# Kernel optimization log

Hardware: AMD Instinct MI355X
Metric: run time of the kernel (lower is better)

Reference implementation:

```python
import jax, jax.numpy as jnp
import numpy as np

N, IN_DIM, HEADS, OUT_DIM = 100000, 128, 4, 32
E = 1600000
NEG_SLOPE = 0.2

def setup_inputs() -> dict:
    key = jax.random.key(0)
    k1, k2, k3, k4, k5 = jax.random.split(key, 5)
    x = jax.random.normal(k1, (N, IN_DIM), dtype=jnp.float32)
    edge_index = jax.random.randint(k2, (2, E), 0, N, dtype=jnp.int32)
    # xavier-like init for params
    W = jax.random.uniform(k3, (IN_DIM, HEADS * OUT_DIM), dtype=jnp.float32,
                           minval=-1.0, maxval=1.0) * np.sqrt(6.0 / (IN_DIM + HEADS * OUT_DIM))
    a_src = jax.random.uniform(k4, (HEADS, OUT_DIM), dtype=jnp.float32,
                               minval=-1.0, maxval=1.0) * np.sqrt(6.0 / (HEADS + OUT_DIM))
    a_dst = jax.random.uniform(k5, (HEADS, OUT_DIM), dtype=jnp.float32,
                               minval=-1.0, maxval=1.0) * np.sqrt(6.0 / (HEADS + OUT_DIM))
    return {"x": x, "edge_index": edge_index, "W": W, "a_src": a_src, "a_dst": a_dst}

def reference(x, edge_index, W, a_src, a_dst):
    src, dst = edge_index[0], edge_index[1]
    n = x.shape[0]
    h = (x @ W).reshape(n, HEADS, OUT_DIM)                      # (N,H,D)
    # per-node attention score halves, then gather per edge (avoids E x D gather twice)
    s_src = jnp.einsum('nhd,hd->nh', h, a_src)                  # (N,H)
    s_dst = jnp.einsum('nhd,hd->nh', h, a_dst)                  # (N,H)
    e = s_src[src] + s_dst[dst]                                 # (E,H)
    e = jnp.where(e > 0, e, NEG_SLOPE * e)                      # leaky_relu(0.2)
    # segment softmax over edges sharing the same dst, per head
    max_per_dst = jax.ops.segment_max(e, dst, num_segments=n)   # (N,H)
    exp = jnp.exp(e - max_per_dst[dst])                         # (E,H)
    denom = jax.ops.segment_sum(exp, dst, num_segments=n)       # (N,H)
    alpha = exp / (denom[dst] + 1e-9)                           # (E,H)
    msg = h[src] * alpha[:, :, None]                            # (E,H,D)
    out = jax.ops.segment_sum(msg, dst, num_segments=n)         # (N,H,D)
    return out.reshape(n, HEADS * OUT_DIM)                      # concat=True
```

## Files before the change

kernel.cpp:

```cpp
#include <hip/hip_runtime.h>
#include <hip/hip_bf16.h>
#include <stdint.h>

#define N_NODES 100000
#define NE 1600000
#define NEG_SLOPE 0.2f
#define NSTRIP 6250
#define NGROUP 49
#define GCAP 34816
#define NFB 64
#define NBKT 3136
#define CAP 768
#define NCTR (NGROUP * 32 + NBKT)

typedef __attribute__((ext_vector_type(8))) short bf16x8;
typedef __attribute__((ext_vector_type(4))) float f32x4;
typedef __attribute__((ext_vector_type(2))) float f32x2;
typedef __attribute__((ext_vector_type(4))) uint32_t u32x4;
typedef __attribute__((ext_vector_type(2))) uint32_t u32x2;

__device__ __forceinline__ short f2bf(float f) {
    __hip_bfloat16 b = __float2bfloat16(f);
    short s; __builtin_memcpy(&s, &b, 2); return s;
}

__global__ __launch_bounds__(256) void k_prep(const float* __restrict__ W,
                                              const float* __restrict__ a_src,
                                              const float* __restrict__ a_dst,
                                              float* __restrict__ vv,
                                              short* __restrict__ wbf,
                                              int* __restrict__ ctrs) {
    const int t = threadIdx.x;
    if (blockIdx.x == 0) {
        if (t < 128) {
            const float* wrow = W + t * 128;
            #pragma unroll
            for (int hd = 0; hd < 4; ++hd) {
                float va = 0.f, vd = 0.f;
                #pragma unroll
                for (int d = 0; d < 32; ++d) {
                    float w = wrow[hd * 32 + d];
                    va += w * a_src[hd * 32 + d];
                    vd += w * a_dst[hd * 32 + d];
                }
                vv[t * 8 + hd]     = va;
                vv[t * 8 + 4 + hd] = vd;
            }
        }
        #pragma unroll 4
        for (int i = 0; i < 64; ++i) {
            int idx = t + i * 256;
            int k = idx >> 7, c = idx & 127;
            int byte = ((c << 8) + (k << 1)) ^ ((c & 7) << 4);
            *(short*)((char*)wbf + byte) = f2bf(W[idx]);
        }
    } else {
        for (int i = t; i < NCTR; i += 256) ctrs[i] = 0;
    }
}

__global__ __launch_bounds__(256) void k_gemm(const float* __restrict__ x,
                                              const short* __restrict__ wbf,
                                              const float* __restrict__ vv,
                                              unsigned char* __restrict__ h8,
                                              float* __restrict__ scales,
                                              float* __restrict__ sv) {
    __shared__ short wt[16384];
    __shared__ float vvl[1024];
    __shared__ float sc[64];
    const int t = threadIdx.x;

    {
        const int4* wsrc = (const int4*)wbf;
        int4* wdst = (int4*)wt;
        #pragma unroll
        for (int i = 0; i < 8; ++i) wdst[t + i * 256] = wsrc[t + i * 256];
    }
    *(f32x4*)(vvl + t * 4) = *(const f32x4*)(vv + t * 4);
    __syncthreads();

    const int wid = t >> 6, lane = t & 63;
    const int strip = blockIdx.x * 4 + wid;
    const bool active = strip < NSTRIP;
    const int r0 = strip * 16;
    const int lr = lane & 15, lg = lane >> 4;

    f32x4 acc[8];
    #pragma unroll
    for (int ct = 0; ct < 8; ++ct) acc[ct] = (f32x4){0.f, 0.f, 0.f, 0.f};
    float part[8];
    #pragma unroll
    for (int i = 0; i < 8; ++i) part[i] = 0.f;

    if (active) {
        bf16x8 a[4];
        #pragma unroll
        for (int kk = 0; kk < 4; ++kk) {
            const float* xp = x + (size_t)(r0 + lr) * 128 + kk * 32 + lg * 8;
            f32x4 x0 = *(const f32x4*)xp;
            f32x4 x1 = *(const f32x4*)(xp + 4);
            int kbase = kk * 32 + lg * 8;
            #pragma unroll
            for (int j = 0; j < 4; ++j) {
                a[kk][j]     = f2bf(x0[j]);
                a[kk][4 + j] = f2bf(x1[j]);
                f32x4 v0 = *(const f32x4*)(vvl + (kbase + j) * 8);
                f32x4 v1 = *(const f32x4*)(vvl + (kbase + j) * 8 + 4);
                f32x4 w0 = *(const f32x4*)(vvl + (kbase + 4 + j) * 8);
                f32x4 w1 = *(const f32x4*)(vvl + (kbase + 4 + j) * 8 + 4);
                #pragma unroll
                for (int i = 0; i < 4; ++i) {
                    part[i]     += x0[j] * v0[i] + x1[j] * w0[i];
                    part[4 + i] += x0[j] * v1[i] + x1[j] * w1[i];
                }
            }
        }
        #pragma unroll
        for (int ct = 0; ct < 8; ++ct) {
            int c = ct * 16 + lr;
            #pragma unroll
            for (int kk = 0; kk < 4; ++kk) {
                int byte = ((c << 8) + ((kk * 32 + lg * 8) << 1)) ^ ((c & 7) << 4);
                bf16x8 b = *(const bf16x8*)((char*)wt + byte);
                acc[ct] = __builtin_amdgcn_mfma_f32_16x16x32_bf16(a[kk], b, acc[ct], 0, 0, 0);
            }
        }
    }
    #pragma unroll
    for (int i = 0; i < 8; ++i) {
        part[i] += __shfl_xor(part[i], 16);
        part[i] += __shfl_xor(part[i], 32);
    }
    if (active && lg == 0) {
        f32x4 s0, s1;
        #pragma unroll
        for (int j = 0; j < 4; ++j) { s0[j] = part[j]; s1[j] = part[4 + j]; }
        *(f32x4*)(sv + (size_t)(r0 + lr) * 8)     = s0;
        *(f32x4*)(sv + (size_t)(r0 + lr) * 8 + 4) = s1;
    }
    if (active) {
        #pragma unroll
        for (int j = 0; j < 4; ++j) {
            float rm = 0.f;
            #pragma unroll
            for (int ct = 0; ct < 8; ++ct) rm = fmaxf(rm, fabsf(acc[ct][j]));
            #pragma unroll
            for (int off2 = 1; off2 < 16; off2 <<= 1)
                rm = fmaxf(rm, __shfl_xor(rm, off2));
            if (lr == 0) {
                scales[r0 + lg * 4 + j] = rm * (1.f / 127.f);
                sc[wid * 16 + lg * 4 + j] = 127.f / fmaxf(rm, 1e-20f);
            }
        }
    }
    __syncthreads();
    if (active) {
        #pragma unroll
        for (int ct = 0; ct < 8; ++ct) {
            #pragma unroll
            for (int j = 0; j < 4; ++j) {
                int row = wid * 16 + lg * 4 + j;
                wt[row * 128 + ct * 16 + lr] = f2bf(acc[ct][j]);
            }
        }
    }
    __syncthreads();
    const int R0 = blockIdx.x * 64;
    #pragma unroll
    for (int it = 0; it < 2; ++it) {
        int sidx = (it * 256 + t) * 16;
        int lrow = sidx >> 7, ch0 = sidx & 127;
        int grow = R0 + lrow;
        if (grow < N_NODES) {
            float invs = sc[lrow];
            u32x4 dws;
            #pragma unroll
            for (int d = 0; d < 4; ++d) {
                uint32_t dw = 0;
                #pragma unroll
                for (int bb = 0; bb < 4; ++bb) {
                    union { uint32_t i; float f; } uu;
                    uu.i = ((uint32_t)(uint16_t)wt[sidx + d * 4 + bb]) << 16;
                    float q = rintf(uu.f * invs);
                    q = fminf(fmaxf(q, -127.f), 127.f);
                    dw |= ((uint32_t)(int)(q + 128.f)) << (8 * bb);
                }
                dws[d] = dw;
            }
            *(u32x4*)(h8 + (size_t)grow * 128 + ch0) = dws;
        }
    }
}

__global__ __launch_bounds__(256) void k_part1(const int* __restrict__ ei,
                                               int* __restrict__ gcur,
                                               int* __restrict__ arena) {
    __shared__ int hist[NGROUP];
    __shared__ int lstart[NGROUP + 1];
    __shared__ int gb[NGROUP];
    __shared__ int binned[4096];
    const int t = threadIdx.x;
    const int e4b = blockIdx.x * 1024;
    if (t < NGROUP) hist[t] = 0;
    __syncthreads();
    int pk[16], gr[16], pl[16];
    #pragma unroll
    for (int i = 0; i < 4; ++i) {
        int e4 = e4b + i * 256 + t;
        bool v = e4 < NE / 4;
        int4 s4 = {0, 0, 0, 0}, d4 = {0, 0, 0, 0};
        if (v) {
            s4 = *(const int4*)(ei + (size_t)e4 * 4);
            d4 = *(const int4*)(ei + NE + (size_t)e4 * 4);
        }
#define P1(k, sf, df) { \
        if (v) { int g = (df) >> 11; gr[i*4+k] = g; \
                 pk[i*4+k] = ((sf) << 11) | ((df) & 2047); \
                 pl[i*4+k] = atomicAdd(&hist[g], 1); } else gr[i*4+k] = -1; }
        P1(0, s4.x, d4.x) P1(1, s4.y, d4.y) P1(2, s4.z, d4.z) P1(3, s4.w, d4.w)
#undef P1
    }
    __syncthreads();
    if (t < 64) {
        int v = (t < NGROUP) ? hist[t] : 0;
        int incl = v;
        #pragma unroll
        for (int off = 1; off < 64; off <<= 1) {
            int y = __shfl_up(incl, off);
            if (t >= off) incl += y;
        }
        if (t < NGROUP) lstart[t + 1] = incl;
        if (t == 0) lstart[0] = 0;
    }
    __syncthreads();
    if (t < NGROUP) gb[t] = atomicAdd(&gcur[t * 32], hist[t]);
    #pragma unroll
    for (int j = 0; j < 16; ++j)
        if (gr[j] >= 0) binned[lstart[gr[j]] + pl[j]] = pk[j];
    __syncthreads();
    const int lane = t & 63, wid = t >> 6;
    for (int g = wid; g < NGROUP; g += 4) {
        int base = gb[g];
        int n = min(hist[g], GCAP - base);
        const int ls = lstart[g];
        int* dst = arena + (size_t)g * GCAP + base;
        for (int i = lane; i < n; i += 64) dst[i] = binned[ls + i];
    }
}

__global__ __launch_bounds__(256) void k_part2(const int* __restrict__ gcur,
                                               const int* __restrict__ arena,
                                               int* __restrict__ bcur,
                                               int* __restrict__ tmp2) {
    const int g = blockIdx.x / 9, chunk = blockIdx.x - g * 9;
    const int cnt = min(gcur[g * 32], GCAP);
    const int cb = chunk * 4096;
    if (cb >= cnt) return;
    __shared__ int hist[NFB];
    __shared__ int lstart[NFB + 1];
    __shared__ int gb[NFB];
    __shared__ int binned[4096];
    const int t = threadIdx.x;
    if (t < NFB) hist[t] = 0;
    __syncthreads();
    int pk[16], fb[16], pl[16];
    const int* ga = arena + (size_t)g * GCAP;
    #pragma unroll
    for (int i = 0; i < 4; ++i) {
        int i4 = cb / 4 + i * 256 + t;
        bool v4 = (i4 * 4) < cnt;
        int4 w4 = {0, 0, 0, 0};
        if (v4) w4 = *(const int4*)(ga + (size_t)i4 * 4);
#define P2(k, wf) { int idx = i4 * 4 + k; \
        if (v4 && idx < cnt) { int f = ((wf) & 2047) >> 5; fb[i*4+k] = f; \
            pk[i*4+k] = (((wf) >> 11) << 5) | ((wf) & 31); \
            pl[i*4+k] = atomicAdd(&hist[f], 1); } else fb[i*4+k] = -1; }
        P2(0, w4.x) P2(1, w4.y) P2(2, w4.z) P2(3, w4.w)
#undef P2
    }
    __syncthreads();
    if (t < 64) {
        int v = hist[t];
        int incl = v;
        #pragma unroll
        for (int off = 1; off < 64; off <<= 1) {
            int y = __shfl_up(incl, off);
            if (t >= off) incl += y;
        }
        lstart[t + 1] = incl;
        if (t == 0) lstart[0] = 0;
    }
    __syncthreads();
    if (t < NFB) gb[t] = atomicAdd(&bcur[g * 64 + t], hist[t]);
    #pragma unroll
    for (int j = 0; j < 16; ++j)
        if (fb[j] >= 0) binned[lstart[fb[j]] + pl[j]] = pk[j];
    __syncthreads();
    const int lane = t & 63, wid = t >> 6;
    for (int f = wid; f < NFB; f += 4) {
        int base = gb[f];
        int n = min(hist[f], CAP - base);
        const int ls = lstart[f];
        int* dst = tmp2 + (size_t)(g * 64 + f) * CAP + base;
        for (int i = lane; i < n; i += 64) dst[i] = binned[ls + i];
    }
}

__global__ __launch_bounds__(256) void k_aggregate(const unsigned char* __restrict__ h8,
                                                   const float* __restrict__ scales,
                                                   const float* __restrict__ sv,
                                                   const int* __restrict__ bcur,
                                                   const int* __restrict__ tmp2,
                                                   float* __restrict__ out) {
    const int b = blockIdx.x;
    const int base = (b >> 6) * 2048 + (b & 63) * 32;
    if (base >= N_NODES) return;
    __shared__ int sorted[CAP];
    __shared__ float wbuf[CAP * 4];
    __shared__ float sbuf[CAP];
    __shared__ int cstart[33];
    __shared__ int ccnt[32];
    __shared__ f32x4 svd4[32];
    const int t = threadIdx.x;
    if (t < 32) {
        ccnt[t] = 0;
        svd4[t] = *(const f32x4*)(sv + (size_t)(base + t) * 8 + 4);
    }
    __syncthreads();
    const int cnt = min(bcur[b], CAP);
    const int* mytmp = tmp2 + (size_t)b * CAP;
    int e0 = -1, e1 = -1, e2 = -1, q0 = 0, q1 = 0, q2 = 0;
    if (t < cnt)       { e0 = mytmp[t];       q0 = atomicAdd(&ccnt[e0 & 31], 1); }
    if (t + 256 < cnt) { e1 = mytmp[t + 256]; q1 = atomicAdd(&ccnt[e1 & 31], 1); }
    if (t + 512 < cnt) { e2 = mytmp[t + 512]; q2 = atomicAdd(&ccnt[e2 & 31], 1); }
    __syncthreads();
    if (t < 64) {
        int v = (t < 32) ? ccnt[t] : 0;
        int incl = v;
        #pragma unroll
        for (int off = 1; off < 32; off <<= 1) {
            int y = __shfl_up(incl, off);
            if (t >= off) incl += y;
        }
        if (t < 32) cstart[t + 1] = incl;
        if (t == 0) cstart[0] = 0;
    }
    __syncthreads();
#define PLACE(e, q) { \
        int pos = cstart[(e) & 31] + (q); \
        sorted[pos] = (e); \
        sbuf[pos] = scales[(size_t)((e) >> 5)]; \
        f32x4 ss = *(const f32x4*)(sv + (size_t)((e) >> 5) * 8); \
        f32x4 sd = svd4[(e) & 31]; \
        f32x4 w4; \
        _Pragma("unroll") \
        for (int hh2 = 0; hh2 < 4; ++hh2) { \
            float v = ss[hh2] + sd[hh2]; \
            v = v > 0.f ? v : NEG_SLOPE * v; \
            w4[hh2] = __expf(v); \
        } \
        *(f32x4*)(wbuf + pos * 4) = w4; }
    if (e0 >= 0) PLACE(e0, q0)
    if (e1 >= 0) PLACE(e1, q1)
    if (e2 >= 0) PLACE(e2, q2)
#undef PLACE
    __syncthreads();

    const int lane = t & 63, wid = t >> 6;
    const int sg = lane >> 4, sl = lane & 15;
    const int hh = sl >> 2;
    const u32x2* hp2 = (const u32x2*)h8;
    #pragma unroll
    for (int r8 = 0; r8 < 8; ++r8) {
        int r = wid * 8 + r8;
        int s0 = cstart[r], s1 = cstart[r + 1];
        f32x2 a01 = {0.f, 0.f}, a23 = {0.f, 0.f};
        f32x2 a45 = {0.f, 0.f}, a67 = {0.f, 0.f};
        float wsum = 0.f, aws = 0.f;
        for (int j = s0 + sg; j < s1; j += 16) {
            int j1 = j + 4, j2 = j + 8, j3 = j + 12;
            int ja = j1 < s1 ? j1 : j;
            int jb = j2 < s1 ? j2 : j;
            int jc = j3 < s1 ? j3 : j;
            int ea = sorted[j], eb = sorted[ja], ec = sorted[jb], ed = sorted[jc];
            float w0 = wbuf[j * 4 + hh];
            float w1 = j1 < s1 ? wbuf[ja * 4 + hh] : 0.f;
            float w2 = j2 < s1 ? wbuf[jb * 4 + hh] : 0.f;
            float w3 = j3 < s1 ? wbuf[jc * 4 + hh] : 0.f;
            float ws0 = w0 * sbuf[j];
            float ws1 = w1 * sbuf[ja];
            float ws2 = w2 * sbuf[jb];
            float ws3 = w3 * sbuf[jc];
            u32x2 p0 = hp2[(size_t)(ea >> 5) * 16 + sl];
            u32x2 p1 = hp2[(size_t)(eb >> 5) * 16 + sl];
            u32x2 p2 = hp2[(size_t)(ec >> 5) * 16 + sl];
            u32x2 p3 = hp2[(size_t)(ed >> 5) * 16 + sl];
#define ACCI(p, ws) { \
            f32x2 ww = {(ws), (ws)}; \
            a01 += ww * (f32x2){(float)((p)[0] & 255u), (float)(((p)[0] >> 8) & 255u)}; \
            a23 += ww * (f32x2){(float)(((p)[0] >> 16) & 255u), (float)((p)[0] >> 24)}; \
            a45 += ww * (f32x2){(float)((p)[1] & 255u), (float)(((p)[1] >> 8) & 255u)}; \
            a67 += ww * (f32x2){(float)(((p)[1] >> 16) & 255u), (float)((p)[1] >> 24)}; }
            ACCI(p0, ws0) ACCI(p1, ws1) ACCI(p2, ws2) ACCI(p3, ws3)
#undef ACCI
            wsum += w0 + w1 + w2 + w3;
            aws  += ws0 + ws1 + ws2 + ws3;
        }
        a01[0] += __shfl_xor(a01[0], 16); a01[0] += __shfl_xor(a01[0], 32);
        a01[1] += __shfl_xor(a01[1], 16); a01[1] += __shfl_xor(a01[1], 32);
        a23[0] += __shfl_xor(a23[0], 16); a23[0] += __shfl_xor(a23[0], 32);
        a23[1] += __shfl_xor(a23[1], 16); a23[1] += __shfl_xor(a23[1], 32);
        a45[0] += __shfl_xor(a45[0], 16); a45[0] += __shfl_xor(a45[0], 32);
        a45[1] += __shfl_xor(a45[1], 16); a45[1] += __shfl_xor(a45[1], 32);
        a67[0] += __shfl_xor(a67[0], 16); a67[0] += __shfl_xor(a67[0], 32);
        a67[1] += __shfl_xor(a67[1], 16); a67[1] += __shfl_xor(a67[1], 32);
        wsum += __shfl_xor(wsum, 16); wsum += __shfl_xor(wsum, 32);
        aws  += __shfl_xor(aws, 16);  aws  += __shfl_xor(aws, 32);
        if (sg == (r8 & 3)) {
            float inv = 1.f / (wsum + 1e-9f);
            float corr = 128.f * aws;
            f32x4 o0 = {(a01[0] - corr) * inv, (a01[1] - corr) * inv,
                        (a23[0] - corr) * inv, (a23[1] - corr) * inv};
            f32x4 o1 = {(a45[0] - corr) * inv, (a45[1] - corr) * inv,
                        (a67[0] - corr) * inv, (a67[1] - corr) * inv};
            float* op = out + (size_t)(base + r) * 128 + sl * 8;
            *(f32x4*)op = o0;
            *(f32x4*)(op + 4) = o1;
        }
    }
}

extern "C" void kernel_launch(void* const* d_in, const int* in_sizes, int n_in,
                              void* d_out, int out_size, void* d_ws, size_t ws_size,
                              hipStream_t stream) {
    const float* x     = (const float*)d_in[0];
    const int*   ei    = (const int*)d_in[1];
    const float* W     = (const float*)d_in[2];
    const float* a_src = (const float*)d_in[3];
    const float* a_dst = (const float*)d_in[4];
    float* out = (float*)d_out;

    char* ws = (char*)d_ws;
    size_t off = 0;
    auto alloc = [&](size_t bytes) {
        char* p = ws + off;
        off += (bytes + 255) & ~(size_t)255;
        return p;
    };
    unsigned char* h8 = (unsigned char*)alloc((size_t)N_NODES * 128);
    float* scales     = (float*)alloc((size_t)N_NODES * 4);
    float* sv         = (float*)alloc((size_t)N_NODES * 8 * 4);
    float* vv         = (float*)alloc(1024 * 4);
    short* wbf        = (short*)alloc(16384 * 2);
    int* ctrs         = (int*)alloc((size_t)NCTR * 4);
    int* tmp2         = (int*)alloc((size_t)NBKT * CAP * 4);
    int* gcur         = ctrs;
    int* bcur         = ctrs + NGROUP * 32;
    int* arena        = (int*)d_out;

    k_prep<<<2, 256, 0, stream>>>(W, a_src, a_dst, vv, wbf, ctrs);
    k_gemm<<<(NSTRIP + 3) / 4, 256, 0, stream>>>(x, wbf, vv, h8, scales, sv);
    k_part1<<<(NE + 4095) / 4096, 256, 0, stream>>>(ei, gcur, arena);
    k_part2<<<NGROUP * 9, 256, 0, stream>>>(gcur, arena, bcur, tmp2);
    k_aggregate<<<NBKT, 256, 0, stream>>>(h8, scales, sv, bcur, tmp2, out);
}
```

Measured before the change: 135.0 us.

## Merge GEMM and edge partition kernels; assign one 16-lane subgroup per destination row

Folds the edge-partition pass and the node GEMM/quantize pass into a single launch, where the first block range does edge binning and the rest does the projection. The two independent phases can then overlap and one launch disappears. The aggregation loop also changes: each 16-lane subgroup now owns two destination rows and walks their edges serially, instead of four subgroups splitting one row's edges. This removes the cross-subgroup shuffle reductions, at the cost of load imbalance on rows with skewed degrees.

```diff
diff --git a/kernel.cpp b/kernel.cpp
--- a/kernel.cpp
+++ b/kernel.cpp
@@ -12,6 +12,7 @@
 #define NBKT 3136
 #define CAP 768
 #define NCTR (NGROUP * 32 + NBKT)
+#define NPB1 391
 
 typedef __attribute__((ext_vector_type(8))) short bf16x8;
 typedef __attribute__((ext_vector_type(4))) float f32x4;
@@ -59,17 +60,75 @@
     }
 }
 
-__global__ __launch_bounds__(256) void k_gemm(const float* __restrict__ x,
-                                              const short* __restrict__ wbf,
-                                              const float* __restrict__ vv,
-                                              unsigned char* __restrict__ h8,
-                                              float* __restrict__ scales,
-                                              float* __restrict__ sv) {
-    __shared__ short wt[16384];
-    __shared__ float vvl[1024];
-    __shared__ float sc[64];
+__global__ __launch_bounds__(256) void k_fused(const float* __restrict__ x,
+                                               const short* __restrict__ wbf,
+                                               const float* __restrict__ vv,
+                                               unsigned char* __restrict__ h8,
+                                               float* __restrict__ scales,
+                                               float* __restrict__ sv,
+                                               const int* __restrict__ ei,
+                                               int* __restrict__ gcur,
+                                               int* __restrict__ arena) {
+    __shared__ int4 smem4[2320];
     const int t = threadIdx.x;
 
+    if (blockIdx.x < NPB1) {
+        int* binned = (int*)smem4;
+        int* hist   = binned + 4096;
+        int* lstart = hist + NGROUP;
+        int* gb     = lstart + NGROUP + 1;
+        const int e4b = blockIdx.x * 1024;
+        if (t < NGROUP) hist[t] = 0;
+        __syncthreads();
+        int pk[16], gr[16], pl[16];
+        #pragma unroll
+        for (int i = 0; i < 4; ++i) {
+            int e4 = e4b + i * 256 + t;
+            bool v = e4 < NE / 4;
+            int4 s4 = {0, 0, 0, 0}, d4 = {0, 0, 0, 0};
+            if (v) {
+                s4 = *(const int4*)(ei + (size_t)e4 * 4);
+                d4 = *(const int4*)(ei + NE + (size_t)e4 * 4);
+            }
+#define P1(k, sf, df) { \
+            if (v) { int g = (df) >> 11; gr[i*4+k] = g; \
+                     pk[i*4+k] = ((sf) << 11) | ((df) & 2047); \
+                     pl[i*4+k] = atomicAdd(&hist[g], 1); } else gr[i*4+k] = -1; }
+            P1(0, s4.x, d4.x) P1(1, s4.y, d4.y) P1(2, s4.z, d4.z) P1(3, s4.w, d4.w)
+#undef P1
+        }
+        __syncthreads();
+        if (t < 64) {
+            int v = (t < NGROUP) ? hist[t] : 0;
+            int incl = v;
+            #pragma unroll
+            for (int off = 1; off < 64; off <<= 1) {
+                int y = __shfl_up(incl, off);
+                if (t >= off) incl += y;
+            }
+            if (t < NGROUP) lstart[t + 1] = incl;
+            if (t == 0) lstart[0] = 0;
+        }
+        __syncthreads();
+        if (t < NGROUP) gb[t] = atomicAdd(&gcur[t * 32], hist[t]);
+        #pragma unroll
+        for (int j = 0; j < 16; ++j)
+            if (gr[j] >= 0) binned[lstart[gr[j]] + pl[j]] = pk[j];
+        __syncthreads();
+        const int lane = t & 63, wid = t >> 6;
+        for (int g = wid; g < NGROUP; g += 4) {
+            int base = gb[g];
+            int n = min(hist[g], GCAP - base);
+            const int ls = lstart[g];
+            int* dst = arena + (size_t)g * GCAP + base;
+            for (int i = lane; i < n; i += 64) dst[i] = binned[ls + i];
+        }
+        return;
+    }
+
+    short* wt  = (short*)smem4;
+    float* vvl = (float*)(smem4 + 2048);
+    float* sc  = (float*)(smem4 + 2304);
     {
         const int4* wsrc = (const int4*)wbf;
         int4* wdst = (int4*)wt;
@@ -80,7 +139,7 @@
     __syncthreads();
 
     const int wid = t >> 6, lane = t & 63;
-    const int strip = blockIdx.x * 4 + wid;
+    const int strip = (blockIdx.x - NPB1) * 4 + wid;
     const bool active = strip < NSTRIP;
     const int r0 = strip * 16;
     const int lr = lane & 15, lg = lane >> 4;
@@ -165,7 +224,7 @@
         }
     }
     __syncthreads();
-    const int R0 = blockIdx.x * 64;
+    const int R0 = (blockIdx.x - NPB1) * 64;
     #pragma unroll
     for (int it = 0; it < 2; ++it) {
         int sidx = (it * 256 + t) * 16;
@@ -189,62 +248,6 @@
             }
             *(u32x4*)(h8 + (size_t)grow * 128 + ch0) = dws;
         }
-    }
-}
-
-__global__ __launch_bounds__(256) void k_part1(const int* __restrict__ ei,
-                                               int* __restrict__ gcur,
-                                               int* __restrict__ arena) {
-    __shared__ int hist[NGROUP];
-    __shared__ int lstart[NGROUP + 1];
-    __shared__ int gb[NGROUP];
-    __shared__ int binned[4096];
-    const int t = threadIdx.x;
-    const int e4b = blockIdx.x * 1024;
-    if (t < NGROUP) hist[t] = 0;
-    __syncthreads();
-    int pk[16], gr[16], pl[16];
-    #pragma unroll
-    for (int i = 0; i < 4; ++i) {
-        int e4 = e4b + i * 256 + t;
-        bool v = e4 < NE / 4;
-        int4 s4 = {0, 0, 0, 0}, d4 = {0, 0, 0, 0};
-        if (v) {
-            s4 = *(const int4*)(ei + (size_t)e4 * 4);
-            d4 = *(const int4*)(ei + NE + (size_t)e4 * 4);
-        }
-#define P1(k, sf, df) { \
-        if (v) { int g = (df) >> 11; gr[i*4+k] = g; \
-                 pk[i*4+k] = ((sf) << 11) | ((df) & 2047); \
-                 pl[i*4+k] = atomicAdd(&hist[g], 1); } else gr[i*4+k] = -1; }
-        P1(0, s4.x, d4.x) P1(1, s4.y, d4.y) P1(2, s4.z, d4.z) P1(3, s4.w, d4.w)
-#undef P1
-    }
-    __syncthreads();
-    if (t < 64) {
-        int v = (t < NGROUP) ? hist[t] : 0;
-        int incl = v;
-        #pragma unroll
-        for (int off = 1; off < 64; off <<= 1) {
-            int y = __shfl_up(incl, off);
-            if (t >= off) incl += y;
-        }
-        if (t < NGROUP) lstart[t + 1] = incl;
-        if (t == 0) lstart[0] = 0;
-    }
-    __syncthreads();
-    if (t < NGROUP) gb[t] = atomicAdd(&gcur[t * 32], hist[t]);
-    #pragma unroll
-    for (int j = 0; j < 16; ++j)
-        if (gr[j] >= 0) binned[lstart[gr[j]] + pl[j]] = pk[j];
-    __syncthreads();
-    const int lane = t & 63, wid = t >> 6;
-    for (int g = wid; g < NGROUP; g += 4) {
-        int base = gb[g];
-        int n = min(hist[g], GCAP - base);
-        const int ls = lstart[g];
-        int* dst = arena + (size_t)g * GCAP + base;
-        for (int i = lane; i < n; i += 64) dst[i] = binned[ls + i];
     }
 }
 
@@ -369,32 +372,32 @@
     const int lane = t & 63, wid = t >> 6;
     const int sg = lane >> 4, sl = lane & 15;
     const int hh = sl >> 2;
+    const int sgid = wid * 4 + sg;
     const u32x2* hp2 = (const u32x2*)h8;
     #pragma unroll
-    for (int r8 = 0; r8 < 8; ++r8) {
-        int r = wid * 8 + r8;
-        int s0 = cstart[r], s1 = cstart[r + 1];
+    for (int rr = 0; rr < 2; ++rr) {
+        const int r = sgid * 2 + rr;
+        const int s0 = cstart[r], s1 = cstart[r + 1];
         f32x2 a01 = {0.f, 0.f}, a23 = {0.f, 0.f};
         f32x2 a45 = {0.f, 0.f}, a67 = {0.f, 0.f};
         float wsum = 0.f, aws = 0.f;
-        for (int j = s0 + sg; j < s1; j += 16) {
-            int j1 = j + 4, j2 = j + 8, j3 = j + 12;
-            int ja = j1 < s1 ? j1 : j;
-            int jb = j2 < s1 ? j2 : j;
-            int jc = j3 < s1 ? j3 : j;
-            int ea = sorted[j], eb = sorted[ja], ec = sorted[jb], ed = sorted[jc];
+        for (int j = s0; j < s1; j += 4) {
+            int j1 = j + 1 < s1 ? j + 1 : j;
+            int j2 = j + 2 < s1 ? j + 2 : j;
+            int j3 = j + 3 < s1 ? j + 3 : j;
+            int eA = sorted[j], eB = sorted[j1], eC = sorted[j2], eD = sorted[j3];
+            u32x2 p0 = hp2[(size_t)(eA >> 5) * 16 + sl];
+            u32x2 p1 = hp2[(size_t)(eB >> 5) * 16 + sl];
+            u32x2 p2 = hp2[(size_t)(eC >> 5) * 16 + sl];
+            u32x2 p3 = hp2[(size_t)(eD >> 5) * 16 + sl];
             float w0 = wbuf[j * 4 + hh];
-            float w1 = j1 < s1 ? wbuf[ja * 4 + hh] : 0.f;
-            float w2 = j2 < s1 ? wbuf[jb * 4 + hh] : 0.f;
-            float w3 = j3 < s1 ? wbuf[jc * 4 + hh] : 0.f;
+            float w1 = j + 1 < s1 ? wbuf[j1 * 4 + hh] : 0.f;
+            float w2 = j + 2 < s1 ? wbuf[j2 * 4 + hh] : 0.f;
+            float w3 = j + 3 < s1 ? wbuf[j3 * 4 + hh] : 0.f;
             float ws0 = w0 * sbuf[j];
-            float ws1 = w1 * sbuf[ja];
-            float ws2 = w2 * sbuf[jb];
-            float ws3 = w3 * sbuf[jc];
-            u32x2 p0 = hp2[(size_t)(ea >> 5) * 16 + sl];
-            u32x2 p1 = hp2[(size_t)(eb >> 5) * 16 + sl];
-            u32x2 p2 = hp2[(size_t)(ec >> 5) * 16 + sl];
-            u32x2 p3 = hp2[(size_t)(ed >> 5) * 16 + sl];
+            float ws1 = w1 * sbuf[j1];
+            float ws2 = w2 * sbuf[j2];
+            float ws3 = w3 * sbuf[j3];
 #define ACCI(p, ws) { \
             f32x2 ww = {(ws), (ws)}; \
             a01 += ww * (f32x2){(float)((p)[0] & 255u), (float)(((p)[0] >> 8) & 255u)}; \
@@ -406,27 +409,13 @@
             wsum += w0 + w1 + w2 + w3;
             aws  += ws0 + ws1 + ws2 + ws3;
         }
-        a01[0] += __shfl_xor(a01[0], 16); a01[0] += __shfl_xor(a01[0], 32);
-        a01[1] += __shfl_xor(a01[1], 16); a01[1] += __shfl_xor(a01[1], 32);
-        a23[0] += __shfl_xor(a23[0], 16); a23[0] += __shfl_xor(a23[0], 32);
-        a23[1] += __shfl_xor(a23[1], 16); a23[1] += __shfl_xor(a23[1], 32);
-        a45[0] += __shfl_xor(a45[0], 16); a45[0] += __shfl_xor(a45[0], 32);
-        a45[1] += __shfl_xor(a45[1], 16); a45[1] += __shfl_xor(a45[1], 32);
-        a67[0] += __shfl_xor(a67[0], 16); a67[0] += __shfl_xor(a67[0], 32);
-        a67[1] += __shfl_xor(a67[1], 16); a67[1] += __shfl_xor(a67[1], 32);
-        wsum += __shfl_xor(wsum, 16); wsum += __shfl_xor(wsum, 32);
-        aws  += __shfl_xor(aws, 16);  aws  += __shfl_xor(aws, 32);
-        if (sg == (r8 & 3)) {
-            float inv = 1.f / (wsum + 1e-9f);
-            float corr = 128.f * aws;
-            f32x4 o0 = {(a01[0] - corr) * inv, (a01[1] - corr) * inv,
-                        (a23[0] - corr) * inv, (a23[1] - corr) * inv};
-            f32x4 o1 = {(a45[0] - corr) * inv, (a45[1] - corr) * inv,
-                        (a67[0] - corr) * inv, (a67[1] - corr) * inv};
-            float* op = out + (size_t)(base + r) * 128 + sl * 8;
-            *(f32x4*)op = o0;
-            *(f32x4*)(op + 4) = o1;
-        }
+        float inv = 1.f / (wsum + 1e-9f);
+        float corr = 128.f * aws;
+        float* op = out + (size_t)(base + r) * 128 + sl * 8;
+        *(f32x4*)op       = (f32x4){(a01[0] - corr) * inv, (a01[1] - corr) * inv,
+                                    (a23[0] - corr) * inv, (a23[1] - corr) * inv};
+        *(f32x4*)(op + 4) = (f32x4){(a45[0] - corr) * inv, (a45[1] - corr) * inv,
+                                    (a67[0] - corr) * inv, (a67[1] - corr) * inv};
     }
 }
 
@@ -459,8 +448,8 @@
     int* arena        = (int*)d_out;
 
     k_prep<<<2, 256, 0, stream>>>(W, a_src, a_dst, vv, wbf, ctrs);
-    k_gemm<<<(NSTRIP + 3) / 4, 256, 0, stream>>>(x, wbf, vv, h8, scales, sv);
-    k_part1<<<(NE + 4095) / 4096, 256, 0, stream>>>(ei, gcur, arena);
+    k_fused<<<NPB1 + (NSTRIP + 3) / 4, 256, 0, stream>>>(x, wbf, vv, h8, scales, sv,
+                                                         ei, gcur, arena);
     k_part2<<<NGROUP * 9, 256, 0, stream>>>(gcur, arena, bcur, tmp2);
     k_aggregate<<<NBKT, 256, 0, stream>>>(h8, scales, sv, bcur, tmp2, out);
 }
```

Result: faster. 126.6 us (-6.3%).
